# Optimization experiments

Measured on AMD Instinct MI355X. Metric: run time of the kernel, lower is better.

Reference implementation:

```python
import jax, jax.numpy as jnp
import numpy as np

D_MODEL = 2048
N_STATE = 256          # power of two
RANK = 64
LEVELS = int(np.log2(N_STATE))  # 8 butterfly levels
B, S = 4, 4096


def setup_inputs() -> dict:
    key = jax.random.key(0)
    ks = jax.random.split(key, 7)
    u = jax.random.normal(ks[0], (B, S, D_MODEL), dtype=jnp.float32)
    # stacked 2x2 butterfly factors, one per level (orthogonal-ish init)
    A_factors = jax.random.normal(ks[1], (LEVELS, 2, 2), dtype=jnp.float32)
    A_factors = A_factors / jnp.linalg.norm(A_factors, axis=-1, keepdims=True)
    W_b_rank = jax.random.normal(ks[2], (D_MODEL, RANK), dtype=jnp.float32) * (1.0 / np.sqrt(D_MODEL))
    W_b_state = jax.random.normal(ks[3], (RANK, N_STATE), dtype=jnp.float32) * (1.0 / np.sqrt(RANK))
    W_c_rank = jax.random.normal(ks[4], (N_STATE, RANK), dtype=jnp.float32) * (1.0 / np.sqrt(N_STATE))
    W_c_model = jax.random.normal(ks[5], (RANK, D_MODEL), dtype=jnp.float32) * (1.0 / np.sqrt(RANK))
    D_vec = jax.random.normal(ks[6], (D_MODEL,), dtype=jnp.float32) * 0.02
    return {"u": u, "A_factors": A_factors, "W_b_rank": W_b_rank,
            "W_b_state": W_b_state, "W_c_rank": W_c_rank,
            "W_c_model": W_c_model, "D_vec": D_vec}


def _apply_butterfly(state, A_factors):
    # state: [B, S, N]; reshape N into LEVELS axes of size 2 and apply a 2x2
    # factor along each axis (contracting the axis with A's FIRST dim, i.e.
    # x @ A, matching tf.matmul(flattened, factor)).
    b, s, n = state.shape
    x = state.reshape((b, s) + (2,) * LEVELS)
    for lvl in range(LEVELS):
        ax = 2 + lvl
        x = jnp.moveaxis(jnp.tensordot(x, A_factors[lvl], axes=[[ax], [0]]), -1, ax)
    return x.reshape(b, s, n)


def reference(u, A_factors, W_b_rank, W_b_state, W_c_rank, W_c_model, D_vec):
    # B path: low-rank projection to state space
    state = (u @ W_b_rank) @ W_b_state              # [B,S,N]
    # A: butterfly-structured state transform
    state = _apply_butterfly(state, A_factors)      # [B,S,N]
    # C path: low-rank projection back to model dim
    y = (state @ W_c_rank) @ W_c_model              # [B,S,D]
    # D: elementwise feedthrough
    return y + D_vec * u
```

## Files before the change

### kernel.cpp

```cpp
#include <hip/hip_runtime.h>

typedef unsigned short ushort_t;
typedef __attribute__((ext_vector_type(8))) short bf16x8;
typedef __attribute__((ext_vector_type(4))) float f32x4;
typedef __attribute__((ext_vector_type(4))) unsigned short us4;

#define DM 2048
#define RK 64
#define MTOT 16384
#define MB 16

__device__ __forceinline__ float b2f(ushort_t v) {
    union { unsigned u; float f; } x; x.u = ((unsigned)v) << 16; return x.f;
}
__device__ __forceinline__ ushort_t f2b(float f) {
    union { float f; unsigned u; } x; x.f = f;
    unsigned r = x.u + 0x7fff + ((x.u >> 16) & 1);
    return (ushort_t)(r >> 16);
}

__global__ void k_bf(const float* __restrict__ Af, float* __restrict__ Bf) {
    __shared__ float A[32];
    if (threadIdx.x < 32) A[threadIdx.x] = Af[threadIdx.x];
    __syncthreads();
    int i = blockIdx.x, j = threadIdx.x;
    float p = 1.0f;
#pragma unroll
    for (int l = 0; l < 8; ++l) {
        int bi = (i >> (7 - l)) & 1;
        int bj = (j >> (7 - l)) & 1;
        p *= A[l * 4 + bi * 2 + bj];
    }
    Bf[i * 256 + j] = p;
}

__global__ void k_t1(const float* __restrict__ Wbs, const float* __restrict__ Bf,
                     float* __restrict__ T1) {
    int r = blockIdx.x, j = threadIdx.x;
    float s = 0.f;
    for (int n = 0; n < 256; ++n) s += Wbs[r * 256 + n] * Bf[n * 256 + j];
    T1[r * 256 + j] = s;
}

__global__ void k_mid(const float* __restrict__ T1, const float* __restrict__ Wcr,
                      float* __restrict__ Mmid) {
    int id = blockIdx.x * 256 + threadIdx.x;
    int r1 = id >> 6, r2 = id & 63;
    float s = 0.f;
    for (int n = 0; n < 256; ++n) s += T1[r1 * 256 + n] * Wcr[n * 64 + r2];
    Mmid[r1 * 64 + r2] = s;
}

__global__ void k_weff(const float* __restrict__ Wbr, const float* __restrict__ Mmid,
                       ushort_t* __restrict__ WeffT) {
    int id = blockIdx.x * 256 + threadIdx.x;
    int n = id >> 11, k = id & 2047;
    float s = 0.f;
#pragma unroll 8
    for (int r = 0; r < 64; ++r) s += Wbr[k * 64 + r] * Mmid[r * 64 + n];
    WeffT[id] = f2b(s);
}

__global__ void k_wct(const float* __restrict__ Wcm, ushort_t* __restrict__ WcT) {
    int id = blockIdx.x * 256 + threadIdx.x;
    int n = id >> 6, k = id & 63;
    WcT[id] = f2b(Wcm[k * 2048 + n]);
}

__global__ __launch_bounds__(256) void k_main(const float* __restrict__ u,
                                              const ushort_t* __restrict__ WeffT,
                                              const ushort_t* __restrict__ WcT,
                                              const float* __restrict__ Dvec,
                                              float* __restrict__ out) {
    __shared__ ushort_t lds[32768];

    const int tid = threadIdx.x;
    const int w = tid >> 6;
    const int lane = tid & 63;
    const int m16 = lane & 15;
    const int quad = lane >> 4;
    const size_t row0 = (size_t)blockIdx.x * MB;
    const float* ub = u + row0 * DM;

#pragma unroll 8
    for (int it = 0; it < 32; ++it) {
        int flat = it * 1024 + tid * 4;
        int r = flat >> 11, c = flat & 2047;
        float4 v = *(const float4*)(ub + flat);
        int phys = r * 2048 + (((c & ~7) ^ ((r & 7) << 3)) | (c & 7));
        us4 o;
        o.x = f2b(v.x); o.y = f2b(v.y); o.z = f2b(v.z); o.w = f2b(v.w);
        *(us4*)&lds[phys] = o;
    }
    __syncthreads();

    f32x4 acc = {0.f, 0.f, 0.f, 0.f};
    const int n0 = w * 16;
    const int swzA = (m16 & 7) << 3;
    const ushort_t* Bp1 = WeffT + (size_t)(n0 + m16) * DM + quad * 8;
#pragma unroll 4
    for (int kk = 0; kk < 64; ++kk) {
        int c8 = kk * 32 + quad * 8;
        bf16x8 a = *(const bf16x8*)&lds[m16 * 2048 + (c8 ^ swzA)];
        bf16x8 b = *(const bf16x8*)(Bp1 + kk * 32);
        acc = __builtin_amdgcn_mfma_f32_16x16x32_bf16(a, b, acc, 0, 0, 0);
    }
    __syncthreads();

#pragma unroll
    for (int i = 0; i < 4; ++i)
        lds[31616 + (quad * 4 + i) * 72 + n0 + m16] = f2b(acc[i]);
    __syncthreads();

    bf16x8 ta0 = *(const bf16x8*)&lds[31616 + m16 * 72 + quad * 8];
    bf16x8 ta1 = *(const bf16x8*)&lds[31616 + m16 * 72 + 32 + quad * 8];

    for (int nt = 0; nt < 32; ++nt) {
        const int n0c = w * 512 + nt * 16;
        const int colc = n0c + m16;
        const ushort_t* Bp = WcT + (size_t)colc * RK + quad * 8;
        bf16x8 b0 = *(const bf16x8*)(Bp);
        bf16x8 b1 = *(const bf16x8*)(Bp + 32);
        f32x4 o = {0.f, 0.f, 0.f, 0.f};
        o = __builtin_amdgcn_mfma_f32_16x16x32_bf16(ta0, b0, o, 0, 0, 0);
        o = __builtin_amdgcn_mfma_f32_16x16x32_bf16(ta1, b1, o, 0, 0, 0);
        const float dv = Dvec[colc];
        const int c8 = n0c + (m16 & 8);
        const int lowc = m16 & 7;
#pragma unroll
        for (int i = 0; i < 4; ++i) {
            int r = quad * 4 + i;
            int phys = r * 2048 + ((c8 ^ ((r & 7) << 3)) | lowc);
            float uv = b2f(lds[phys]);
            if (r == 15 && colc >= 896)
                uv = ub[15 * 2048 + colc];
            out[(row0 + r) * DM + colc] = o[i] + dv * uv;
        }
    }
}

extern "C" void kernel_launch(void* const* d_in, const int* in_sizes, int n_in,
                              void* d_out, int out_size, void* d_ws, size_t ws_size,
                              hipStream_t stream) {
    const float* u   = (const float*)d_in[0];
    const float* Af  = (const float*)d_in[1];
    const float* Wbr = (const float*)d_in[2];
    const float* Wbs = (const float*)d_in[3];
    const float* Wcr = (const float*)d_in[4];
    const float* Wcm = (const float*)d_in[5];
    const float* Dv  = (const float*)d_in[6];
    float* out = (float*)d_out;

    char* ws = (char*)d_ws;
    float*    Bf    = (float*)(ws + 0);
    float*    T1    = (float*)(ws + 262144);
    float*    Mmid  = (float*)(ws + 327680);
    ushort_t* WeffT = (ushort_t*)(ws + 344064);
    ushort_t* WcT   = (ushort_t*)(ws + 606208);

    k_bf  <<<256, 256, 0, stream>>>(Af, Bf);
    k_t1  <<< 64, 256, 0, stream>>>(Wbs, Bf, T1);
    k_mid <<< 16, 256, 0, stream>>>(T1, Wcr, Mmid);
    k_weff<<<512, 256, 0, stream>>>(Wbr, Mmid, WeffT);
    k_wct <<<512, 256, 0, stream>>>(Wcm, WcT);
    k_main<<<MTOT / MB, 256, 0, stream>>>(u, WeffT, WcT, Dv, out);
}
```

Measured before the change: 335.5 us.

## Fuse weight precompute kernels and restructure main kernel with split-K waves

After: 327.2 us. 2.5% less time.

```diff
diff --git a/kernel.cpp b/kernel.cpp
--- a/kernel.cpp
+++ b/kernel.cpp
@@ -7,141 +7,202 @@
 
 #define DM 2048
 #define RK 64
-#define MTOT 16384
-#define MB 16
-
-__device__ __forceinline__ float b2f(ushort_t v) {
-    union { unsigned u; float f; } x; x.u = ((unsigned)v) << 16; return x.f;
-}
+
 __device__ __forceinline__ ushort_t f2b(float f) {
     union { float f; unsigned u; } x; x.f = f;
     unsigned r = x.u + 0x7fff + ((x.u >> 16) & 1);
     return (ushort_t)(r >> 16);
 }
 
-__global__ void k_bf(const float* __restrict__ Af, float* __restrict__ Bf) {
-    __shared__ float A[32];
-    if (threadIdx.x < 32) A[threadIdx.x] = Af[threadIdx.x];
+__global__ void k_p1(const float* __restrict__ Wbs, const float* __restrict__ Af,
+                     const float* __restrict__ Wcr, float* __restrict__ Mmid) {
+    __shared__ float X[64 * 256];
+    const int tid = threadIdx.x;
+
+#pragma unroll
+    for (int i = 0; i < 16; ++i) {
+        int e = (i * 256 + tid) * 4;
+        *(float4*)&X[e] = *(const float4*)&Wbs[e];
+    }
     __syncthreads();
-    int i = blockIdx.x, j = threadIdx.x;
-    float p = 1.0f;
+
 #pragma unroll
     for (int l = 0; l < 8; ++l) {
-        int bi = (i >> (7 - l)) & 1;
-        int bj = (j >> (7 - l)) & 1;
-        p *= A[l * 4 + bi * 2 + bj];
-    }
-    Bf[i * 256 + j] = p;
-}
-
-__global__ void k_t1(const float* __restrict__ Wbs, const float* __restrict__ Bf,
-                     float* __restrict__ T1) {
-    int r = blockIdx.x, j = threadIdx.x;
-    float s = 0.f;
-    for (int n = 0; n < 256; ++n) s += Wbs[r * 256 + n] * Bf[n * 256 + j];
-    T1[r * 256 + j] = s;
-}
-
-__global__ void k_mid(const float* __restrict__ T1, const float* __restrict__ Wcr,
-                      float* __restrict__ Mmid) {
-    int id = blockIdx.x * 256 + threadIdx.x;
-    int r1 = id >> 6, r2 = id & 63;
-    float s = 0.f;
-    for (int n = 0; n < 256; ++n) s += T1[r1 * 256 + n] * Wcr[n * 64 + r2];
-    Mmid[r1 * 64 + r2] = s;
-}
-
-__global__ void k_weff(const float* __restrict__ Wbr, const float* __restrict__ Mmid,
-                       ushort_t* __restrict__ WeffT) {
-    int id = blockIdx.x * 256 + threadIdx.x;
-    int n = id >> 11, k = id & 2047;
+        const int bit = 1 << (7 - l);
+        const float a00 = Af[l * 4 + 0], a01 = Af[l * 4 + 1];
+        const float a10 = Af[l * 4 + 2], a11 = Af[l * 4 + 3];
+#pragma unroll 4
+        for (int p = 0; p < 32; ++p) {
+            int pid = p * 256 + tid;
+            int row = pid >> 7;
+            int off = pid & 127;
+            int lo = off & (bit - 1);
+            int n0 = ((off ^ lo) << 1) | lo;
+            int n1 = n0 | bit;
+            float x0 = X[row * 256 + n0], x1 = X[row * 256 + n1];
+            X[row * 256 + n0] = x0 * a00 + x1 * a10;
+            X[row * 256 + n1] = x0 * a01 + x1 * a11;
+        }
+        __syncthreads();
+    }
+
+    int g = blockIdx.x * 256 + tid;
+    int r1 = g >> 6, r2 = g & 63;
     float s = 0.f;
 #pragma unroll 8
-    for (int r = 0; r < 64; ++r) s += Wbr[k * 64 + r] * Mmid[r * 64 + n];
-    WeffT[id] = f2b(s);
-}
-
-__global__ void k_wct(const float* __restrict__ Wcm, ushort_t* __restrict__ WcT) {
-    int id = blockIdx.x * 256 + threadIdx.x;
-    int n = id >> 6, k = id & 63;
-    WcT[id] = f2b(Wcm[k * 2048 + n]);
-}
-
-__global__ __launch_bounds__(256) void k_main(const float* __restrict__ u,
-                                              const ushort_t* __restrict__ WeffT,
-                                              const ushort_t* __restrict__ WcT,
-                                              const float* __restrict__ Dvec,
-                                              float* __restrict__ out) {
-    __shared__ ushort_t lds[32768];
+    for (int n = 0; n < 256; ++n) s += X[r1 * 256 + n] * Wcr[n * 64 + r2];
+    Mmid[g] = s;
+}
+
+__global__ void k_p2(const float* __restrict__ Wbr, const float* __restrict__ Mmid,
+                     const float* __restrict__ Wcm,
+                     ushort_t* __restrict__ WeffT, ushort_t* __restrict__ WcT) {
+    const int b = blockIdx.x, tid = threadIdx.x;
+    if (b < 32) {
+        __shared__ float LW[64][65];
+        __shared__ float LM[64 * 64];
+#pragma unroll
+        for (int i = 0; i < 4; ++i) {
+            int e = (i * 256 + tid) * 4;
+            int kk = e >> 6, r = e & 63;
+            float4 v = *(const float4*)&Wbr[(size_t)b * 4096 + e];
+            LW[kk][r] = v.x; LW[kk][r + 1] = v.y; LW[kk][r + 2] = v.z; LW[kk][r + 3] = v.w;
+        }
+#pragma unroll
+        for (int i = 0; i < 4; ++i) {
+            int e = (i * 256 + tid) * 4;
+            *(float4*)&LM[e] = *(const float4*)&Mmid[e];
+        }
+        __syncthreads();
+
+        int kk = tid & 63, n0 = (tid >> 6) * 16;
+        float acc[16];
+#pragma unroll
+        for (int j = 0; j < 16; ++j) acc[j] = 0.f;
+        for (int r = 0; r < 64; ++r) {
+            float wv = LW[kk][r];
+            const float* mrow = &LM[r * 64 + n0];
+            float4 m0 = *(const float4*)(mrow);
+            float4 m1 = *(const float4*)(mrow + 4);
+            float4 m2 = *(const float4*)(mrow + 8);
+            float4 m3 = *(const float4*)(mrow + 12);
+            acc[0] += wv * m0.x; acc[1] += wv * m0.y; acc[2] += wv * m0.z; acc[3] += wv * m0.w;
+            acc[4] += wv * m1.x; acc[5] += wv * m1.y; acc[6] += wv * m1.z; acc[7] += wv * m1.w;
+            acc[8] += wv * m2.x; acc[9] += wv * m2.y; acc[10] += wv * m2.z; acc[11] += wv * m2.w;
+            acc[12] += wv * m3.x; acc[13] += wv * m3.y; acc[14] += wv * m3.z; acc[15] += wv * m3.w;
+        }
+#pragma unroll
+        for (int j = 0; j < 16; ++j)
+            WeffT[(size_t)(n0 + j) * DM + b * 64 + kk] = f2b(acc[j]);
+    } else {
+        __shared__ float LT[64][65];
+        const int n0 = (b - 32) * 64;
+#pragma unroll
+        for (int i = 0; i < 4; ++i) {
+            int e = (i * 256 + tid) * 4;
+            int k = e >> 6, nn = e & 63;
+            float4 v = *(const float4*)&Wcm[(size_t)k * DM + n0 + nn];
+            LT[k][nn] = v.x; LT[k][nn + 1] = v.y; LT[k][nn + 2] = v.z; LT[k][nn + 3] = v.w;
+        }
+        __syncthreads();
+#pragma unroll
+        for (int i = 0; i < 4; ++i) {
+            int e = (i * 256 + tid) * 4;
+            int nn = e >> 6, k = e & 63;
+            us4 o;
+            o.x = f2b(LT[k][nn]); o.y = f2b(LT[k + 1][nn]);
+            o.z = f2b(LT[k + 2][nn]); o.w = f2b(LT[k + 3][nn]);
+            *(us4*)&WcT[(size_t)(n0 + nn) * RK + k] = o;
+        }
+    }
+}
+
+__global__ __launch_bounds__(512, 5) void k_main(const float* __restrict__ u,
+                                                 const ushort_t* __restrict__ WeffT,
+                                                 const ushort_t* __restrict__ WcT,
+                                                 const float* __restrict__ Dvec,
+                                                 float* __restrict__ out) {
+    __shared__ float red[8][64][20];
+    __shared__ ushort_t tsh[16 * 72];
 
     const int tid = threadIdx.x;
     const int w = tid >> 6;
     const int lane = tid & 63;
     const int m16 = lane & 15;
     const int quad = lane >> 4;
-    const size_t row0 = (size_t)blockIdx.x * MB;
+    const size_t row0 = (size_t)blockIdx.x * 16;
     const float* ub = u + row0 * DM;
 
-#pragma unroll 8
-    for (int it = 0; it < 32; ++it) {
-        int flat = it * 1024 + tid * 4;
-        int r = flat >> 11, c = flat & 2047;
-        float4 v = *(const float4*)(ub + flat);
-        int phys = r * 2048 + (((c & ~7) ^ ((r & 7) << 3)) | (c & 7));
-        us4 o;
-        o.x = f2b(v.x); o.y = f2b(v.y); o.z = f2b(v.z); o.w = f2b(v.w);
-        *(us4*)&lds[phys] = o;
-    }
+    f32x4 acc0 = {0.f, 0.f, 0.f, 0.f}, acc1 = acc0, acc2 = acc0, acc3 = acc0;
+    const float* ap = ub + m16 * DM + w * 256 + quad * 8;
+    const ushort_t* bp0 = WeffT + (size_t)m16 * DM + w * 256 + quad * 8;
+#pragma unroll 4
+    for (int ks = 0; ks < 8; ++ks) {
+        const int k0 = ks * 32;
+        float4 u0 = *(const float4*)(ap + k0);
+        float4 u1 = *(const float4*)(ap + k0 + 4);
+        bf16x8 a;
+        a[0] = (short)f2b(u0.x); a[1] = (short)f2b(u0.y);
+        a[2] = (short)f2b(u0.z); a[3] = (short)f2b(u0.w);
+        a[4] = (short)f2b(u1.x); a[5] = (short)f2b(u1.y);
+        a[6] = (short)f2b(u1.z); a[7] = (short)f2b(u1.w);
+        bf16x8 b0 = *(const bf16x8*)(bp0 + k0);
+        bf16x8 b1 = *(const bf16x8*)(bp0 + 16 * DM + k0);
+        bf16x8 b2 = *(const bf16x8*)(bp0 + 32 * DM + k0);
+        bf16x8 b3 = *(const bf16x8*)(bp0 + 48 * DM + k0);
+        acc0 = __builtin_amdgcn_mfma_f32_16x16x32_bf16(a, b0, acc0, 0, 0, 0);
+        acc1 = __builtin_amdgcn_mfma_f32_16x16x32_bf16(a, b1, acc1, 0, 0, 0);
+        acc2 = __builtin_amdgcn_mfma_f32_16x16x32_bf16(a, b2, acc2, 0, 0, 0);
+        acc3 = __builtin_amdgcn_mfma_f32_16x16x32_bf16(a, b3, acc3, 0, 0, 0);
+    }
+    *(f32x4*)&red[w][ 0 + m16][quad * 4] = acc0;
+    *(f32x4*)&red[w][16 + m16][quad * 4] = acc1;
+    *(f32x4*)&red[w][32 + m16][quad * 4] = acc2;
+    *(f32x4*)&red[w][48 + m16][quad * 4] = acc3;
     __syncthreads();
 
-    f32x4 acc = {0.f, 0.f, 0.f, 0.f};
-    const int n0 = w * 16;
-    const int swzA = (m16 & 7) << 3;
-    const ushort_t* Bp1 = WeffT + (size_t)(n0 + m16) * DM + quad * 8;
-#pragma unroll 4
-    for (int kk = 0; kk < 64; ++kk) {
-        int c8 = kk * 32 + quad * 8;
-        bf16x8 a = *(const bf16x8*)&lds[m16 * 2048 + (c8 ^ swzA)];
-        bf16x8 b = *(const bf16x8*)(Bp1 + kk * 32);
-        acc = __builtin_amdgcn_mfma_f32_16x16x32_bf16(a, b, acc, 0, 0, 0);
+    {
+        const int n = tid >> 3, r2 = (tid & 7) * 2;
+        float s0 = 0.f, s1 = 0.f;
+#pragma unroll
+        for (int ww = 0; ww < 8; ++ww) {
+            float2 v = *(const float2*)&red[ww][n][r2];
+            s0 += v.x; s1 += v.y;
+        }
+        tsh[r2 * 72 + n]       = f2b(s0);
+        tsh[(r2 + 1) * 72 + n] = f2b(s1);
     }
     __syncthreads();
 
-#pragma unroll
-    for (int i = 0; i < 4; ++i)
-        lds[31616 + (quad * 4 + i) * 72 + n0 + m16] = f2b(acc[i]);
-    __syncthreads();
-
-    bf16x8 ta0 = *(const bf16x8*)&lds[31616 + m16 * 72 + quad * 8];
-    bf16x8 ta1 = *(const bf16x8*)&lds[31616 + m16 * 72 + 32 + quad * 8];
-
-    for (int nt = 0; nt < 32; ++nt) {
-        const int n0c = w * 512 + nt * 16;
-        const int colc = n0c + m16;
-        const ushort_t* Bp = WcT + (size_t)colc * RK + quad * 8;
-        bf16x8 b0 = *(const bf16x8*)(Bp);
-        bf16x8 b1 = *(const bf16x8*)(Bp + 32);
+    bf16x8 ta0 = *(const bf16x8*)&tsh[m16 * 72 + quad * 8];
+    bf16x8 ta1 = *(const bf16x8*)&tsh[m16 * 72 + 32 + quad * 8];
+    const ushort_t* wcb = WcT + (size_t)(w * 256 + m16) * RK + quad * 8;
+    const float* u2 = ub + m16 * DM + w * 256 + quad * 4;
+    const float* dp = Dvec + w * 256 + quad * 4;
+    float* op = out + (row0 + m16) * DM + w * 256 + quad * 4;
+#pragma unroll 2
+    for (int nt = 0; nt < 16; ++nt) {
+        const ushort_t* bp2 = wcb + nt * 16 * RK;
+        bf16x8 wb0 = *(const bf16x8*)(bp2);
+        bf16x8 wb1 = *(const bf16x8*)(bp2 + 32);
         f32x4 o = {0.f, 0.f, 0.f, 0.f};
-        o = __builtin_amdgcn_mfma_f32_16x16x32_bf16(ta0, b0, o, 0, 0, 0);
-        o = __builtin_amdgcn_mfma_f32_16x16x32_bf16(ta1, b1, o, 0, 0, 0);
-        const float dv = Dvec[colc];
-        const int c8 = n0c + (m16 & 8);
-        const int lowc = m16 & 7;
-#pragma unroll
-        for (int i = 0; i < 4; ++i) {
-            int r = quad * 4 + i;
-            int phys = r * 2048 + ((c8 ^ ((r & 7) << 3)) | lowc);
-            float uv = b2f(lds[phys]);
-            if (r == 15 && colc >= 896)
-                uv = ub[15 * 2048 + colc];
-            out[(row0 + r) * DM + colc] = o[i] + dv * uv;
-        }
+        o = __builtin_amdgcn_mfma_f32_16x16x32_bf16(wb0, ta0, o, 0, 0, 0);
+        o = __builtin_amdgcn_mfma_f32_16x16x32_bf16(wb1, ta1, o, 0, 0, 0);
+        float4 uv = *(const float4*)(u2 + nt * 16);
+        float4 dv = *(const float4*)(dp + nt * 16);
+        f32x4 st;
+        st.x = o[0] + dv.x * uv.x;
+        st.y = o[1] + dv.y * uv.y;
+        st.z = o[2] + dv.z * uv.z;
+        st.w = o[3] + dv.w * uv.w;
+        __builtin_nontemporal_store(st, (f32x4*)(op + nt * 16));
     }
 }
 
 extern "C" void kernel_launch(void* const* d_in, const int* in_sizes, int n_in,
                               void* d_out, int out_size, void* d_ws, size_t ws_size,
                               hipStream_t stream) {
+    (void)in_sizes; (void)n_in; (void)out_size; (void)ws_size;
     const float* u   = (const float*)d_in[0];
     const float* Af  = (const float*)d_in[1];
     const float* Wbr = (const float*)d_in[2];
@@ -152,16 +213,11 @@
     float* out = (float*)d_out;
 
     char* ws = (char*)d_ws;
-    float*    Bf    = (float*)(ws + 0);
-    float*    T1    = (float*)(ws + 262144);
-    float*    Mmid  = (float*)(ws + 327680);
-    ushort_t* WeffT = (ushort_t*)(ws + 344064);
-    ushort_t* WcT   = (ushort_t*)(ws + 606208);
-
-    k_bf  <<<256, 256, 0, stream>>>(Af, Bf);
-    k_t1  <<< 64, 256, 0, stream>>>(Wbs, Bf, T1);
-    k_mid <<< 16, 256, 0, stream>>>(T1, Wcr, Mmid);
-    k_weff<<<512, 256, 0, stream>>>(Wbr, Mmid, WeffT);
-    k_wct <<<512, 256, 0, stream>>>(Wcm, WcT);
-    k_main<<<MTOT / MB, 256, 0, stream>>>(u, WeffT, WcT, Dv, out);
-}
+    float*    Mmid  = (float*)(ws + 0);
+    ushort_t* WeffT = (ushort_t*)(ws + 16384);
+    ushort_t* WcT   = (ushort_t*)(ws + 278528);
+
+    k_p1<<<16, 256, 0, stream>>>(Wbs, Af, Wcr, Mmid);
+    k_p2<<<64, 256, 0, stream>>>(Wbr, Mmid, Wcm, WeffT, WcT);
+    k_main<<<1024, 512, 0, stream>>>(u, WeffT, WcT, Dv, out);
+}
```
